# Kernel tuning notes

Measured on AMD Instinct MI355X. Metric: run time of the kernel, lower is better.

The kernel has to match this reference:

```python
import jax, jax.numpy as jnp
import numpy as np

N = 8192
D_IN = 6       # dim(concat(node, centre)) = 3 + 3
D_OUT = 512    # output_size


def setup_inputs() -> dict:
    key = jax.random.key(0)
    ks = jax.random.split(key, 9)
    s_in = 1.0 / np.sqrt(D_IN)
    s_v = 1.0 / np.sqrt(2 * D_OUT)
    return {
        "nodes": jax.random.normal(ks[0], (N, 3), dtype=jnp.float32),
        "centre": jax.random.normal(ks[1], (1, 3), dtype=jnp.float32),
        "Wq": jax.random.uniform(ks[2], (D_OUT, D_IN), jnp.float32, -s_in, s_in),
        "bq": jax.random.uniform(ks[3], (D_OUT,), jnp.float32, -s_in, s_in),
        "Wk": jax.random.uniform(ks[4], (D_OUT, D_IN), jnp.float32, -s_in, s_in),
        "bk": jax.random.uniform(ks[5], (D_OUT,), jnp.float32, -s_in, s_in),
        "Wv": jax.random.uniform(ks[6], (D_OUT, 2 * D_OUT), jnp.float32, -s_v, s_v),
        "bv": jax.random.uniform(ks[7], (D_OUT,), jnp.float32, -s_v, s_v),
    }


def reference(nodes, centre, Wq, bq, Wk, bk, Wv, bv):
    n = nodes.shape[0]
    d = Wv.shape[0]
    # x = concat(nodes, broadcast centre)  -> [N, 6]
    x = jnp.concatenate([nodes, jnp.broadcast_to(centre, (n, centre.shape[1]))], axis=1)
    keys = x @ Wk.T + bk          # [N, D]
    queries = x @ Wq.T + bq       # [N, D]
    attn = jax.nn.softmax(keys @ queries.T, axis=1)  # [N, N], rows sum to 1
    # values(concat(queries, keys[n])) decomposes linearly:
    #   V[n, m] = queries[m] @ Wv_q.T + keys[n] @ Wv_k.T + bv
    # so out[n] = attn[n] @ (queries @ Wv_q.T) + keys[n] @ Wv_k.T + bv
    Wv_q = Wv[:, :d]
    Wv_k = Wv[:, d:]
    out = attn @ (queries @ Wv_q.T) + keys @ Wv_k.T + bv
    return keys + out
```

## Files before the change

kernel.cpp:

```cpp
#include <hip/hip_runtime.h>

typedef unsigned int u32;

#define N_NODES 8192
#define DOUT    512
#define LOG2E   1.4426950408889634f
#define SQRT3   1.7320508075688772f


__global__ __launch_bounds__(64) void k2_tables_aux(
    const float* __restrict__ nodes, const float* __restrict__ centre,
    const float* __restrict__ Wq, const float* __restrict__ bq,
    const float* __restrict__ Wk, const float* __restrict__ bk,
    const float* __restrict__ Wv, const float* __restrict__ bv,
    float* __restrict__ T, float* __restrict__ aux)
{
    const int r = blockIdx.x, lane = threadIdx.x;
    const float c0 = centre[0], c1 = centre[1], c2 = centre[2];

    if (r < 512) {
        const float* wvq = Wv + (size_t)r * 1024;
        const float* wvk = wvq + 512;

        float m0=0.f,m1=0.f,m2=0.f,uc=0.f,r0=0.f,r1=0.f,r2=0.f,rc=0.f;
        for (int s = lane; s < 512; s += 64) {
            float a = wvq[s];
            float b = wvk[s];
            float kcs = fmaf(Wk[s*6+3], c0, fmaf(Wk[s*6+4], c1,
                        fmaf(Wk[s*6+5], c2, bk[s])));
            float us  = fmaf(Wq[s*6+3], c0, fmaf(Wq[s*6+4], c1,
                        fmaf(Wq[s*6+5], c2, bq[s])));
            m0 = fmaf(a, Wq[s*6+0], m0);
            m1 = fmaf(a, Wq[s*6+1], m1);
            m2 = fmaf(a, Wq[s*6+2], m2);
            uc = fmaf(a, us, uc);
            r0 = fmaf(b, Wk[s*6+0], r0);
            r1 = fmaf(b, Wk[s*6+1], r1);
            r2 = fmaf(b, Wk[s*6+2], r2);
            rc = fmaf(b, kcs, rc);
        }
        #pragma unroll
        for (int off = 32; off; off >>= 1) {
            m0 += __shfl_xor(m0, off); m1 += __shfl_xor(m1, off);
            m2 += __shfl_xor(m2, off); uc += __shfl_xor(uc, off);
            r0 += __shfl_xor(r0, off); r1 += __shfl_xor(r1, off);
            r2 += __shfl_xor(r2, off); rc += __shfl_xor(rc, off);
        }
        if (lane == 0) {
            float kcr = fmaf(Wk[r*6+3], c0, fmaf(Wk[r*6+4], c1,
                        fmaf(Wk[r*6+5], c2, bk[r])));
            T[r*8+0] = Wk[r*6+0] + r0;
            T[r*8+1] = Wk[r*6+1] + r1;
            T[r*8+2] = Wk[r*6+2] + r2;
            T[r*8+3] = kcr + rc + uc + bv[r];
            T[r*8+4] = m0; T[r*8+5] = m1; T[r*8+6] = m2; T[r*8+7] = 0.f;
        }
    } else if (r < 524) {
        const int o = r - 512;
        float acc = 0.f;
        if (o < 9) {
            int a = o / 3, b = o - a*3;
            for (int s = lane; s < 512; s += 64)
                acc = fmaf(Wq[s*6+a], Wk[s*6+b], acc);
        } else {
            int a = o - 9;
            for (int s = lane; s < 512; s += 64) {
                float kc = fmaf(Wk[s*6+3], c0, fmaf(Wk[s*6+4], c1,
                           fmaf(Wk[s*6+5], c2, bk[s])));
                acc = fmaf(Wq[s*6+a], kc, acc);
            }
        }
        #pragma unroll
        for (int off = 32; off; off >>= 1) acc += __shfl_xor(acc, off);
        if (lane == 0) aux[o] = acc * LOG2E;
    } else {
        const int b = r - 524;
        const float4* src = (const float4*)nodes + (size_t)b * 768;
        float m = 0.f;
        for (int k = lane; k < 768; k += 64) {
            float4 v = src[k];
            m = fmaxf(m, fmaxf(fmaxf(fabsf(v.x), fabsf(v.y)),
                               fmaxf(fabsf(v.z), fabsf(v.w))));
        }
        #pragma unroll
        for (int off = 32; off; off >>= 1) m = fmaxf(m, __shfl_xor(m, off));
        if (lane == 0) aux[12 + b] = m;
    }
}

__global__ __launch_bounds__(256) void k3_attn(
    const float* __restrict__ nodes,
    const float* __restrict__ aux, const float* __restrict__ T,
    float* __restrict__ out)
{
    __shared__ float lds[4096 * 3];
    const int tid = threadIdx.x, lane = tid & 63, wv = tid >> 6;
    const int ibase = (blockIdx.x * 4 + wv) * 4;

    const float G00=aux[0],G01=aux[1],G02=aux[2];
    const float G10=aux[3],G11=aux[4],G12=aux[5];
    const float G20=aux[6],G21=aux[7],G22=aux[8];
    const float g0=aux[9],g1=aux[10],g2=aux[11];
    float C = aux[12];
    #pragma unroll
    for (int b = 1; b < 8; ++b) C = fmaxf(C, aux[12+b]);
    const float Nbound = SQRT3 * C;

    float nx_[4], ny_[4], nz_[4], vx[4], vy[4], vz[4], bb[4];
    float S[4], ax[4], ay[4], az[4];
    #pragma unroll
    for (int q = 0; q < 4; ++q) {
        int i = ibase + q;
        float x = nodes[3*i], y = nodes[3*i+1], z = nodes[3*i+2];
        nx_[q]=x; ny_[q]=y; nz_[q]=z;
        float a = fmaf(G00,x, fmaf(G01,y, fmaf(G02,z, g0)));
        float b = fmaf(G10,x, fmaf(G11,y, fmaf(G12,z, g1)));
        float c = fmaf(G20,x, fmaf(G21,y, fmaf(G22,z, g2)));
        vx[q]=a; vy[q]=b; vz[q]=c;
        bb[q] = -sqrtf(fmaf(a,a, fmaf(b,b, c*c))) * Nbound;
        S[q]=0.f; ax[q]=0.f; ay[q]=0.f; az[q]=0.f;
    }

    for (int tile = 0; tile < 2; ++tile) {
        const float4* src = (const float4*)(nodes + tile*12288);
        float4* dst = (float4*)lds;
        for (int k = tid; k < 3072; k += 256) dst[k] = src[k];
        __syncthreads();
        for (int jj = lane; jj < 4096; jj += 64) {
            float nx = lds[jj*3+0], ny = lds[jj*3+1], nz = lds[jj*3+2];
            #pragma unroll
            for (int q = 0; q < 4; ++q) {
                float arg = fmaf(vx[q],nx, fmaf(vy[q],ny, fmaf(vz[q],nz, bb[q])));
                float e = exp2f(arg);
                S[q] += e;
                ax[q] = fmaf(e, nx, ax[q]);
                ay[q] = fmaf(e, ny, ay[q]);
                az[q] = fmaf(e, nz, az[q]);
            }
        }
        __syncthreads();
    }

    #pragma unroll
    for (int q = 0; q < 4; ++q) {
        #pragma unroll
        for (int off = 32; off; off >>= 1) {
            S[q]  += __shfl_xor(S[q],  off);
            ax[q] += __shfl_xor(ax[q], off);
            ay[q] += __shfl_xor(ay[q], off);
            az[q] += __shfl_xor(az[q], off);
        }
        float inv = 1.f / fmaxf(S[q], 1e-35f);
        ax[q] *= inv; ay[q] *= inv; az[q] *= inv;
    }

    const float4* T4 = (const float4*)T;
    #pragma unroll
    for (int t = 0; t < 4; ++t) {
        int d0 = t*128 + lane*2;
        float4 A0 = T4[2*d0+0], B0 = T4[2*d0+1];
        float4 A1 = T4[2*d0+2], B1 = T4[2*d0+3];
        #pragma unroll
        for (int q = 0; q < 4; ++q) {
            float v0 = fmaf(A0.x,nx_[q], fmaf(A0.y,ny_[q], fmaf(A0.z,nz_[q],
                       fmaf(B0.x,ax[q], fmaf(B0.y,ay[q], fmaf(B0.z,az[q], A0.w))))));
            float v1 = fmaf(A1.x,nx_[q], fmaf(A1.y,ny_[q], fmaf(A1.z,nz_[q],
                       fmaf(B1.x,ax[q], fmaf(B1.y,ay[q], fmaf(B1.z,az[q], A1.w))))));
            *(float2*)(out + (size_t)(ibase+q)*DOUT + d0) = make_float2(v0, v1);
        }
    }
}

extern "C" void kernel_launch(void* const* d_in, const int* in_sizes, int n_in,
                              void* d_out, int out_size, void* d_ws, size_t ws_size,
                              hipStream_t stream) {
    const float* nodes  = (const float*)d_in[0];
    const float* centre = (const float*)d_in[1];
    const float* Wq     = (const float*)d_in[2];
    const float* bq     = (const float*)d_in[3];
    const float* Wk     = (const float*)d_in[4];
    const float* bk     = (const float*)d_in[5];
    const float* Wv     = (const float*)d_in[6];
    const float* bv     = (const float*)d_in[7];

    float* ws  = (float*)(((uintptr_t)d_ws + 255) & ~(uintptr_t)255);
    float* aux = ws;
    float* T   = ws + 32;
    float* out = (float*)d_out;

    hipLaunchKernelGGL(k2_tables_aux, dim3(532), dim3(64), 0, stream,
                       nodes, centre, Wq, bq, Wk, bk, Wv, bv, T, aux);
    hipLaunchKernelGGL(k3_attn,       dim3(512), dim3(256), 0, stream,
                       nodes, aux, T, out);
}
```

Measured before the change: 109.5 us.

## Fuse table-setup and attention kernels into one cooperative launch with grid sync

Merges the precompute kernel (T table, aux Gram terms, node max-abs) and the attention kernel into a single cooperative kernel. Different waves of each block do the precompute roles, then a grid-wide sync precedes the attention phase. This removes one kernel launch and the inter-kernel gap. In exchange it requires all 512 blocks to be co-resident and pays for a grid barrier.

Measured after the change: 161.1 us. 1.47x slower.

```diff
diff --git a/kernel.cpp b/kernel.cpp
--- a/kernel.cpp
+++ b/kernel.cpp
@@ -1,31 +1,34 @@
 #include <hip/hip_runtime.h>
+#include <hip/hip_cooperative_groups.h>
 
-typedef unsigned int u32;
+namespace cg = cooperative_groups;
 
 #define N_NODES 8192
 #define DOUT    512
 #define LOG2E   1.4426950408889634f
 #define SQRT3   1.7320508075688772f
 
-
-__global__ __launch_bounds__(64) void k2_tables_aux(
+__global__ __launch_bounds__(256) void k_fused(
     const float* __restrict__ nodes, const float* __restrict__ centre,
     const float* __restrict__ Wq, const float* __restrict__ bq,
     const float* __restrict__ Wk, const float* __restrict__ bk,
     const float* __restrict__ Wv, const float* __restrict__ bv,
-    float* __restrict__ T, float* __restrict__ aux)
+    float* __restrict__ T, float* __restrict__ aux,
+    float* __restrict__ out)
 {
-    const int r = blockIdx.x, lane = threadIdx.x;
+    __shared__ float lds[4096 * 3];
+    const int tid = threadIdx.x, lane = tid & 63, wv = tid >> 6;
+    const int b = blockIdx.x;
     const float c0 = centre[0], c1 = centre[1], c2 = centre[2];
 
-    if (r < 512) {
-        const float* wvq = Wv + (size_t)r * 1024;
+    if (wv == 0) {
+        const float* wvq = Wv + (size_t)b * 1024;
         const float* wvk = wvq + 512;
 
         float m0=0.f,m1=0.f,m2=0.f,uc=0.f,r0=0.f,r1=0.f,r2=0.f,rc=0.f;
         for (int s = lane; s < 512; s += 64) {
             float a = wvq[s];
-            float b = wvk[s];
+            float bb = wvk[s];
             float kcs = fmaf(Wk[s*6+3], c0, fmaf(Wk[s*6+4], c1,
                         fmaf(Wk[s*6+5], c2, bk[s])));
             float us  = fmaf(Wq[s*6+3], c0, fmaf(Wq[s*6+4], c1,
@@ -34,10 +37,10 @@
             m1 = fmaf(a, Wq[s*6+1], m1);
             m2 = fmaf(a, Wq[s*6+2], m2);
             uc = fmaf(a, us, uc);
-            r0 = fmaf(b, Wk[s*6+0], r0);
-            r1 = fmaf(b, Wk[s*6+1], r1);
-            r2 = fmaf(b, Wk[s*6+2], r2);
-            rc = fmaf(b, kcs, rc);
+            r0 = fmaf(bb, Wk[s*6+0], r0);
+            r1 = fmaf(bb, Wk[s*6+1], r1);
+            r2 = fmaf(bb, Wk[s*6+2], r2);
+            rc = fmaf(bb, kcs, rc);
         }
         #pragma unroll
         for (int off = 32; off; off >>= 1) {
@@ -47,21 +50,21 @@
             r2 += __shfl_xor(r2, off); rc += __shfl_xor(rc, off);
         }
         if (lane == 0) {
-            float kcr = fmaf(Wk[r*6+3], c0, fmaf(Wk[r*6+4], c1,
-                        fmaf(Wk[r*6+5], c2, bk[r])));
-            T[r*8+0] = Wk[r*6+0] + r0;
-            T[r*8+1] = Wk[r*6+1] + r1;
-            T[r*8+2] = Wk[r*6+2] + r2;
-            T[r*8+3] = kcr + rc + uc + bv[r];
-            T[r*8+4] = m0; T[r*8+5] = m1; T[r*8+6] = m2; T[r*8+7] = 0.f;
+            float kcr = fmaf(Wk[b*6+3], c0, fmaf(Wk[b*6+4], c1,
+                        fmaf(Wk[b*6+5], c2, bk[b])));
+            T[b*8+0] = Wk[b*6+0] + r0;
+            T[b*8+1] = Wk[b*6+1] + r1;
+            T[b*8+2] = Wk[b*6+2] + r2;
+            T[b*8+3] = kcr + rc + uc + bv[b];
+            T[b*8+4] = m0; T[b*8+5] = m1; T[b*8+6] = m2; T[b*8+7] = 0.f;
         }
-    } else if (r < 524) {
-        const int o = r - 512;
+    } else if (wv == 1 && b < 12) {
+        const int o = b;
         float acc = 0.f;
         if (o < 9) {
-            int a = o / 3, b = o - a*3;
+            int a = o / 3, c = o - a*3;
             for (int s = lane; s < 512; s += 64)
-                acc = fmaf(Wq[s*6+a], Wk[s*6+b], acc);
+                acc = fmaf(Wq[s*6+a], Wk[s*6+c], acc);
         } else {
             int a = o - 9;
             for (int s = lane; s < 512; s += 64) {
@@ -73,8 +76,7 @@
         #pragma unroll
         for (int off = 32; off; off >>= 1) acc += __shfl_xor(acc, off);
         if (lane == 0) aux[o] = acc * LOG2E;
-    } else {
-        const int b = r - 524;
+    } else if (wv == 2 && b < 8) {
         const float4* src = (const float4*)nodes + (size_t)b * 768;
         float m = 0.f;
         for (int k = lane; k < 768; k += 64) {
@@ -86,16 +88,10 @@
         for (int off = 32; off; off >>= 1) m = fmaxf(m, __shfl_xor(m, off));
         if (lane == 0) aux[12 + b] = m;
     }
-}
 
-__global__ __launch_bounds__(256) void k3_attn(
-    const float* __restrict__ nodes,
-    const float* __restrict__ aux, const float* __restrict__ T,
-    float* __restrict__ out)
-{
-    __shared__ float lds[4096 * 3];
-    const int tid = threadIdx.x, lane = tid & 63, wv = tid >> 6;
-    const int ibase = (blockIdx.x * 4 + wv) * 4;
+    cg::this_grid().sync();
+
+    const int ibase = (b * 4 + wv) * 4;
 
     const float G00=aux[0],G01=aux[1],G02=aux[2];
     const float G10=aux[3],G11=aux[4],G12=aux[5];
@@ -103,7 +99,7 @@
     const float g0=aux[9],g1=aux[10],g2=aux[11];
     float C = aux[12];
     #pragma unroll
-    for (int b = 1; b < 8; ++b) C = fmaxf(C, aux[12+b]);
+    for (int p = 1; p < 8; ++p) C = fmaxf(C, aux[12+p]);
     const float Nbound = SQRT3 * C;
 
     float nx_[4], ny_[4], nz_[4], vx[4], vy[4], vz[4], bb[4];
@@ -114,10 +110,10 @@
         float x = nodes[3*i], y = nodes[3*i+1], z = nodes[3*i+2];
         nx_[q]=x; ny_[q]=y; nz_[q]=z;
         float a = fmaf(G00,x, fmaf(G01,y, fmaf(G02,z, g0)));
-        float b = fmaf(G10,x, fmaf(G11,y, fmaf(G12,z, g1)));
+        float bq_ = fmaf(G10,x, fmaf(G11,y, fmaf(G12,z, g1)));
         float c = fmaf(G20,x, fmaf(G21,y, fmaf(G22,z, g2)));
-        vx[q]=a; vy[q]=b; vz[q]=c;
-        bb[q] = -sqrtf(fmaf(a,a, fmaf(b,b, c*c))) * Nbound;
+        vx[q]=a; vy[q]=bq_; vz[q]=c;
+        bb[q] = -sqrtf(fmaf(a,a, fmaf(bq_,bq_, c*c))) * Nbound;
         S[q]=0.f; ax[q]=0.f; ay[q]=0.f; az[q]=0.f;
     }
 
@@ -188,8 +184,9 @@
     float* T   = ws + 32;
     float* out = (float*)d_out;
 
-    hipLaunchKernelGGL(k2_tables_aux, dim3(532), dim3(64), 0, stream,
-                       nodes, centre, Wq, bq, Wk, bk, Wv, bv, T, aux);
-    hipLaunchKernelGGL(k3_attn,       dim3(512), dim3(256), 0, stream,
-                       nodes, aux, T, out);
+    void* args[] = { (void*)&nodes, (void*)&centre, (void*)&Wq, (void*)&bq,
+                     (void*)&Wk, (void*)&bk, (void*)&Wv, (void*)&bv,
+                     (void*)&T, (void*)&aux, (void*)&out };
+    hipLaunchCooperativeKernel((void*)k_fused, dim3(512), dim3(256),
+                               args, 0, stream);
 }
```
